# Performance work log

Hardware: AMD Instinct MI355X
Metric: run time of the kernel (lower is better)

Reference implementation:

```python
import jax, jax.numpy as jnp
import numpy as np


def setup_inputs() -> dict:
    key = jax.random.key(0)
    k0, k1, k2, k3 = jax.random.split(key, 4)
    T, B, K, L, DEG = 2000, 2048, 64, 64, 3
    return {
        "currents": jax.random.normal(k0, (T, B), dtype=jnp.float32),
        "a": jax.random.normal(k1, (K,), dtype=jnp.float32) * 0.05,
        "b_lag": jax.random.normal(k2, (L,), dtype=jnp.float32) * 1e-3,
        "poly_coeff": jax.random.normal(k3, (1, DEG + 1), dtype=jnp.float32) * 0.3,
        "b_act": jnp.zeros((1,), dtype=jnp.float32),
        "max_current": jnp.full((1,), 100.0, dtype=jnp.float32),
        "max_firing_rate": jnp.full((1,), 100.0, dtype=jnp.float32),
    }


def _poly_act(z, poly_coeff, b_act, max_current, max_firing_rate):
    # PolynomialActivation.forward: x=(z-b)/max_current; poly=sum_d x^d * coeff_d^2
    x = (z - b_act[0]) / max_current[0]  # [B]
    deg = poly_coeff.shape[1] - 1
    coeff = (poly_coeff ** 2)[0]  # [deg+1]
    # build integer powers safely (negative bases) via repeated multiply
    pows = [jnp.ones_like(x)]
    for _ in range(deg):
        pows.append(pows[-1] * x)
    powers = jnp.stack(pows, axis=-1)  # [B, deg+1]
    poly = powers @ coeff  # [B]
    return jax.nn.relu(max_firing_rate[0] * jnp.tanh(poly))


def reference(currents, a, b_lag, poly_coeff, b_act, max_current, max_firing_rate):
    T, B = currents.shape
    K, L = a.shape[0], b_lag.shape[0]

    def step(carry, c_t):
        cur_buf, fs_buf = carry  # [B,K], [B,L]
        cur_buf = jnp.concatenate([cur_buf[:, 1:], c_t[:, None]], axis=1)
        x = cur_buf @ a                      # einsum('j,ij->i')
        y = 1000.0 * (fs_buf @ b_lag)        # einsum('j,ij->i')
        f = _poly_act(x + y, poly_coeff, b_act, max_current, max_firing_rate)
        fs_buf = jnp.concatenate([fs_buf[:, 1:], f[:, None]], axis=1)
        return (cur_buf, fs_buf), f

    init = (jnp.zeros((B, K), currents.dtype), jnp.zeros((B, L), currents.dtype))
    _, fs = jax.lax.scan(step, init, currents)  # fs: [T, B]
    return fs
```

## Files before the change

kernel.cpp:

```cpp
#include <hip/hip_runtime.h>

#define T_STEPS 2000
#define BATCH   2048

__global__ __launch_bounds__(256) void fused_kernel(
    const float* __restrict__ currents, const float* __restrict__ a,
    const float* __restrict__ b_lag, const float* __restrict__ poly_coeff,
    const float* __restrict__ b_act, const float* __restrict__ max_current,
    const float* __restrict__ max_firing_rate, float* __restrict__ out)
{
    int tid  = threadIdx.x;
    int lane = tid & 63;
    int wid  = tid >> 6;
    int b    = blockIdx.x * 4 + wid;

    float inv = 1.0f / max_current[0];
    float cba = -b_act[0] * inv;
    float af  = a[63 - lane] * inv;
    float gam = (1000.0f * inv) * b_lag[63 - lane];

    float c0 = poly_coeff[0], c1 = poly_coeff[1], c2 = poly_coeff[2], c3 = poly_coeff[3];
    float k0 = c0*c0, k1 = c1*c1, k2 = c2*c2, k3 = c3*c3;
    float M  = max_firing_rate[0];
    float c105M = 105.0f * M, c945M = 945.0f * M;

    auto bcast = [](float v, int l) {
        return __builtin_bit_cast(float,
            __builtin_amdgcn_readlane(__builtin_bit_cast(int, v), l));
    };
    auto rotl1 = [](float v) {
        int i = __builtin_bit_cast(int, v);
        return __builtin_bit_cast(float,
            __builtin_amdgcn_update_dpp(i, i, 0x134, 0xf, 0xf, false));
    };

    const float* ccol   = currents + b;
    float*       outcol = out + b;

    float R  = cba;
    float cv = ccol[(long)lane * BATCH];
    float fv = 0.0f;

    auto step = [&](int s) {
        float c = bcast(cv, s);
        R = fmaf(af, c, R);
        float u = bcast(R, 0);
        float u2 = u * u;
        float a1 = fmaf(u, k1, k0);
        float a2 = fmaf(u, k3, k2);
        float p  = fmaf(u2, a2, a1);
        float z  = p * p;
        float z2 = z * z;
        float dn = fmaf(z2, 15.0f, fmaf(z, 420.0f, 945.0f));
        float nm = p * fmaf(z, fmaf(z, M, c105M), c945M);
        float r  = __builtin_bit_cast(float,
                       0x7EF311C2 - __builtin_bit_cast(int, dn));
        r = r * fmaf(-dn, r, 2.0f);
        r = r * fmaf(-dn, r, 2.0f);
        float f  = __builtin_amdgcn_fmed3f(nm * r, 0.0f, M);
        float Rr = rotl1(R);
        Rr = (lane == 63) ? cba : Rr;
        R  = fmaf(gam, f, Rr);
        fv = (lane == s) ? f : fv;
    };

    for (int chunk = 0; chunk < 31; ++chunk) {
        int t0 = chunk * 64;
        int tp = t0 + 64 + lane;
        float cv_next = (tp < T_STEPS) ? ccol[(long)tp * BATCH] : 0.0f;
#pragma unroll
        for (int s = 0; s < 64; ++s) step(s);
        outcol[(long)(t0 + lane) * BATCH] = fv;
        cv = cv_next;
    }
#pragma unroll
    for (int s = 0; s < 16; ++s) step(s);
    if (lane < 16) outcol[(long)(1984 + lane) * BATCH] = fv;
}

extern "C" void kernel_launch(void* const* d_in, const int* in_sizes, int n_in,
                              void* d_out, int out_size, void* d_ws, size_t ws_size,
                              hipStream_t stream) {
    const float* currents   = (const float*)d_in[0];
    const float* a          = (const float*)d_in[1];
    const float* b_lag      = (const float*)d_in[2];
    const float* poly_coeff = (const float*)d_in[3];
    const float* b_act      = (const float*)d_in[4];
    const float* mc         = (const float*)d_in[5];
    const float* mfr        = (const float*)d_in[6];
    float* out = (float*)d_out;

    fused_kernel<<<BATCH / 4, 256, 0, stream>>>(
        currents, a, b_lag, poly_coeff, b_act, mc, mfr, out);
}
```

Before: 244.0 us.

## Pack two batch columns per wavefront with 32-lane two-slot lag recurrence

Each batch column now uses 32 lanes that each hold two lag slots (even/odd registers A/B), so one wave64 serves two columns and the grid halves. The per-step critical path is shortened: the broadcast of the next partial sum is issued one step early via ds_swizzle, and the two most recent current and firing contributions are added directly instead of waiting on the rotated accumulator. Currents are loaded directly per step in groups of eight rather than broadcast from lanes with readlane. The risks are more VALU work per lane, ds_swizzle latency, and lower occupancy from launch_bounds(256,1) with fewer blocks.

```diff
diff --git a/kernel.cpp b/kernel.cpp
--- a/kernel.cpp
+++ b/kernel.cpp
@@ -3,48 +3,61 @@
 #define T_STEPS 2000
 #define BATCH   2048
 
-__global__ __launch_bounds__(256) void fused_kernel(
+__device__ __forceinline__ float rol1(float v) {
+    int i = __builtin_bit_cast(int, v);
+    return __builtin_bit_cast(float,
+        __builtin_amdgcn_update_dpp(i, i, 0x134, 0xf, 0xf, false));
+}
+__device__ __forceinline__ float bcast0(float v) {
+    return __builtin_bit_cast(float,
+        __builtin_amdgcn_ds_swizzle(__builtin_bit_cast(int, v), 0x0000));
+}
+
+__global__ __launch_bounds__(256, 1) void fused_kernel(
     const float* __restrict__ currents, const float* __restrict__ a,
     const float* __restrict__ b_lag, const float* __restrict__ poly_coeff,
     const float* __restrict__ b_act, const float* __restrict__ max_current,
     const float* __restrict__ max_firing_rate, float* __restrict__ out)
 {
     int tid  = threadIdx.x;
-    int lane = tid & 63;
-    int wid  = tid >> 6;
-    int b    = blockIdx.x * 4 + wid;
+    int r    = tid & 31;
+    long col = (long)blockIdx.x * 8 + (tid >> 5);
 
     float inv = 1.0f / max_current[0];
+    float g   = 1000.0f * inv;
     float cba = -b_act[0] * inv;
-    float af  = a[63 - lane] * inv;
-    float gam = (1000.0f * inv) * b_lag[63 - lane];
+
+    float af0  = a[63] * inv;
+    float af1  = a[62] * inv;
+    float gam1 = g * b_lag[63];
+    float AFe  = a[63 - (2*r + 1)] * inv;
+    float GAMe = g * b_lag[64 - (2*r + 1)];
+    float AFo  = (r < 31) ? a[63 - (2*r + 2)] * inv : 0.0f;
+    float GAMo = g * b_lag[64 - (2*r + 2)];
 
     float c0 = poly_coeff[0], c1 = poly_coeff[1], c2 = poly_coeff[2], c3 = poly_coeff[3];
     float k0 = c0*c0, k1 = c1*c1, k2 = c2*c2, k3 = c3*c3;
     float M  = max_firing_rate[0];
     float c105M = 105.0f * M, c945M = 945.0f * M;
 
-    auto bcast = [](float v, int l) {
-        return __builtin_bit_cast(float,
-            __builtin_amdgcn_readlane(__builtin_bit_cast(int, v), l));
-    };
-    auto rotl1 = [](float v) {
-        int i = __builtin_bit_cast(int, v);
-        return __builtin_bit_cast(float,
-            __builtin_amdgcn_update_dpp(i, i, 0x134, 0xf, 0xf, false));
-    };
+    bool nb = (r == 31);
 
-    const float* ccol   = currents + b;
-    float*       outcol = out + b;
+    const float* cp = currents + col;
+    float*       op = out + col;
 
-    float R  = cba;
-    float cv = ccol[(long)lane * BATCH];
-    float fv = 0.0f;
+    float A = cba, B = cba;
+    float bc = cba;
+    float f  = 0.0f, cprev = 0.0f, fv = 0.0f;
 
-    auto step = [&](int s) {
-        float c = bcast(cv, s);
-        R = fmaf(af, c, R);
-        float u = bcast(R, 0);
+    float xc[8], xn[8];
+#pragma unroll
+    for (int i = 0; i < 8; ++i) xc[i] = cp[(long)i * BATCH];
+
+    auto STEP = [&](int par, int s, float c) {
+        float bcn = bcast0(par ? A : B);
+        float u = fmaf(af1, cprev, bc);
+        u = fmaf(af0, c, u);
+        u = fmaf(gam1, f, u);
         float u2 = u * u;
         float a1 = fmaf(u, k1, k0);
         float a2 = fmaf(u, k3, k2);
@@ -53,29 +66,51 @@
         float z2 = z * z;
         float dn = fmaf(z2, 15.0f, fmaf(z, 420.0f, 945.0f));
         float nm = p * fmaf(z, fmaf(z, M, c105M), c945M);
-        float r  = __builtin_bit_cast(float,
+        float rc = __builtin_bit_cast(float,
                        0x7EF311C2 - __builtin_bit_cast(int, dn));
-        r = r * fmaf(-dn, r, 2.0f);
-        r = r * fmaf(-dn, r, 2.0f);
-        float f  = __builtin_amdgcn_fmed3f(nm * r, 0.0f, M);
-        float Rr = rotl1(R);
-        Rr = (lane == 63) ? cba : Rr;
-        R  = fmaf(gam, f, Rr);
-        fv = (lane == s) ? f : fv;
+        rc = rc * fmaf(-dn, rc, 2.0f);
+        rc = rc * fmaf(-dn, rc, 2.0f);
+        float fn = __builtin_amdgcn_fmed3f(nm * rc, 0.0f, M);
+        fv = (r == s) ? fn : fv;
+        float sh = rol1(par ? B : A);
+        sh = nb ? cba : sh;
+        sh = fmaf(AFo, c, sh);
+        sh = fmaf(GAMo, fn, sh);
+        float ns = fmaf(AFe, c, par ? A : B);
+        ns = fmaf(GAMe, fn, ns);
+        if (par) { B = sh; A = ns; } else { A = sh; B = ns; }
+        f = fn; cprev = c; bc = bcn;
     };
 
-    for (int chunk = 0; chunk < 31; ++chunk) {
-        int t0 = chunk * 64;
-        int tp = t0 + 64 + lane;
-        float cv_next = (tp < T_STEPS) ? ccol[(long)tp * BATCH] : 0.0f;
+    for (int ch = 0; ch < 62; ++ch) {
+        int t0 = ch * 32;
 #pragma unroll
-        for (int s = 0; s < 64; ++s) step(s);
-        outcol[(long)(t0 + lane) * BATCH] = fv;
-        cv = cv_next;
+        for (int gg = 0; gg < 4; ++gg) {
+            int tf = t0 + gg * 8 + 8;
+#pragma unroll
+            for (int i = 0; i < 8; ++i)
+                xn[i] = cp[(long)(tf + i) * BATCH];
+#pragma unroll
+            for (int i = 0; i < 8; ++i)
+                STEP((gg * 8 + i) & 1, gg * 8 + i, xc[i]);
+#pragma unroll
+            for (int i = 0; i < 8; ++i) xc[i] = xn[i];
+        }
+        op[(long)(t0 + r) * BATCH] = fv;
     }
 #pragma unroll
-    for (int s = 0; s < 16; ++s) step(s);
-    if (lane < 16) outcol[(long)(1984 + lane) * BATCH] = fv;
+    for (int gg = 0; gg < 2; ++gg) {
+        int tf = 1984 + gg * 8 + 8;
+#pragma unroll
+        for (int i = 0; i < 8; ++i)
+            xn[i] = (tf + i < T_STEPS) ? cp[(long)(tf + i) * BATCH] : 0.0f;
+#pragma unroll
+        for (int i = 0; i < 8; ++i)
+            STEP((gg * 8 + i) & 1, gg * 8 + i, xc[i]);
+#pragma unroll
+        for (int i = 0; i < 8; ++i) xc[i] = xn[i];
+    }
+    if (r < 16) op[(long)(1984 + r) * BATCH] = fv;
 }
 
 extern "C" void kernel_launch(void* const* d_in, const int* in_sizes, int n_in,
@@ -90,6 +125,6 @@
     const float* mfr        = (const float*)d_in[6];
     float* out = (float*)d_out;
 
-    fused_kernel<<<BATCH / 4, 256, 0, stream>>>(
+    fused_kernel<<<BATCH / 8, 256, 0, stream>>>(
         currents, a, b_lag, poly_coeff, b_act, mc, mfr, out);
 }
```

New measurement: 219.6 us. 10.0% less time.
